# Optimization experiments

Hardware: AMD Instinct MI355X
Metric: run time of the kernel (lower is better)

The kernel has to match this reference:

```python
import jax, jax.numpy as jnp
import numpy as np

D_MODEL = 1024
N_HEADS = 16
HEAD_DIM = D_MODEL // N_HEADS


def setup_inputs() -> dict:
    key = jax.random.key(0)
    ks = jax.random.split(key, 5)
    s = 1.0 / np.sqrt(D_MODEL)
    return {
        "x": jax.random.normal(ks[0], (2, 2048, D_MODEL), dtype=jnp.float32),
        "w_qkv": jax.random.uniform(ks[1], (3 * D_MODEL, D_MODEL), jnp.float32, -s, s),
        "b_qkv": jax.random.uniform(ks[2], (3 * D_MODEL,), jnp.float32, -s, s),
        "w_out": jax.random.uniform(ks[3], (D_MODEL, D_MODEL), jnp.float32, -s, s),
        "b_out": jax.random.uniform(ks[4], (D_MODEL,), jnp.float32, -s, s),
    }


def _attn(x, w_qkv, b_qkv, w_out, b_out):
    bsz, seq_len, _ = x.shape
    qkv = jnp.einsum('bsd,ed->bse', x, w_qkv) + b_qkv  # [B,S,3D]
    q, k, v = jnp.split(qkv, 3, axis=-1)
    def heads(t):  # [B,S,D] -> [B,H,S,Dh]
        return t.reshape(bsz, seq_len, N_HEADS, HEAD_DIM).transpose(0, 2, 1, 3)
    q, k, v = heads(q), heads(k), heads(v)
    scores = jnp.einsum('bhqd,bhkd->bhqk', q, k) / np.sqrt(HEAD_DIM)
    mask = jnp.tril(jnp.ones((seq_len, seq_len), dtype=bool))
    scores = jnp.where(mask, scores, -jnp.inf)
    probs = jax.nn.softmax(scores, axis=-1)
    attn = jnp.einsum('bhqk,bhkd->bhqd', probs, v)
    attn = attn.transpose(0, 2, 1, 3).reshape(bsz, seq_len, D_MODEL)
    return jnp.einsum('bsd,ed->bse', attn, w_out) + b_out


def reference(x, w_qkv, b_qkv, w_out, b_out):
    return _attn(x, w_qkv, b_qkv, w_out, b_out)
```

## Files before the change

kernel.cpp:

```cpp
#include <hip/hip_runtime.h>
#include <hip/hip_bf16.h>
#include <stdint.h>

#define SEQ     2048
#define BATCH   2
#define NHEADS  16
#define HDIM    64
#define DMODEL  1024
#define N3      3072
#define D2      2048
#define MTOT    (BATCH*SEQ)

typedef __attribute__((ext_vector_type(4))) float f32x4;
typedef __attribute__((ext_vector_type(8))) short bf16x8;

static __device__ inline unsigned short f2bf(float f) {
    union { float f; unsigned u; } v; v.f = f;
    unsigned r = (v.u + 0x7fffu + ((v.u >> 16) & 1u)) >> 16;
    return (unsigned short)r;
}

#define GLDS(gp, lp) __builtin_amdgcn_global_load_lds( \
    (const __attribute__((address_space(1))) void*)(gp), \
    (__attribute__((address_space(3))) void*)(lp), 16, 0, 0)

__global__ void cast_all(const float* __restrict__ x,
                         const float* __restrict__ wqkv,
                         const float* __restrict__ wout,
                         unsigned short* __restrict__ xb,
                         unsigned short* __restrict__ wqkvb,
                         unsigned short* __restrict__ woutb) {
    long i4 = (long)(blockIdx.x * blockDim.x + threadIdx.x) * 4;
    const float* src; unsigned short* dst; long off;
    if (i4 < 4194304L)      { src = x;    dst = xb;    off = i4; }
    else if (i4 < 7340032L) { src = wqkv; dst = wqkvb; off = i4 - 4194304L; }
    else                    { src = wout; dst = woutb; off = i4 - 7340032L; }
    float4 v = *(const float4*)(src + off);
    ushort4 o;
    o.x = f2bf(v.x); o.y = f2bf(v.y); o.z = f2bf(v.z); o.w = f2bf(v.w);
    *(ushort4*)(dst + off) = o;
}

#define BK 32

__global__ __launch_bounds__(256, 2) void gemm_qkv(
    const unsigned short* __restrict__ A,
    const unsigned short* __restrict__ B,
    const float* __restrict__ bias,
    unsigned short* __restrict__ qk,
    unsigned short* __restrict__ vT)
{
    __shared__ __align__(16) unsigned short sA[2][128][BK];
    __shared__ __align__(16) unsigned short sB[2][128][BK];
    const int tid  = threadIdx.x;
    const int wave = tid >> 6, lane = tid & 63;
    const int quad = lane >> 4, l16 = lane & 15;
    const int wm = wave >> 1, wn = wave & 1;
    const int m0 = blockIdx.x * 128, n0 = blockIdx.y * 128;

    f32x4 acc[4][4];
    const f32x4 zero = {0.f, 0.f, 0.f, 0.f};
    #pragma unroll
    for (int i = 0; i < 4; i++)
        #pragma unroll
        for (int j = 0; j < 4; j++) acc[i][j] = zero;

    const unsigned short* gA0 = A + (long)(m0 + (tid >> 2)) * 1024 + (tid & 3) * 8;
    const unsigned short* gB0 = B + (long)(n0 + (tid >> 2)) * 1024 + (tid & 3) * 8;

    GLDS(gA0,               &sA[0][wave * 16][0]);
    GLDS(gA0 + 64L * 1024,  &sA[0][64 + wave * 16][0]);
    GLDS(gB0,               &sB[0][wave * 16][0]);
    GLDS(gB0 + 64L * 1024,  &sB[0][64 + wave * 16][0]);

    int buf = 0;
    for (int k0 = 0; k0 < 1024; k0 += BK, buf ^= 1) {
        __syncthreads();
        if (k0 + BK < 1024) {
            const unsigned short* ga = gA0 + k0 + BK;
            const unsigned short* gb = gB0 + k0 + BK;
            GLDS(ga,              &sA[buf ^ 1][wave * 16][0]);
            GLDS(ga + 64L * 1024, &sA[buf ^ 1][64 + wave * 16][0]);
            GLDS(gb,              &sB[buf ^ 1][wave * 16][0]);
            GLDS(gb + 64L * 1024, &sB[buf ^ 1][64 + wave * 16][0]);
        }
        bf16x8 af[4], bfr[4];
        #pragma unroll
        for (int mt = 0; mt < 4; mt++)
            af[mt] = *(const bf16x8*)(&sA[buf][wm * 64 + mt * 16 + l16][quad * 8]);
        #pragma unroll
        for (int nt = 0; nt < 4; nt++)
            bfr[nt] = *(const bf16x8*)(&sB[buf][wn * 64 + nt * 16 + l16][quad * 8]);
        #pragma unroll
        for (int mt = 0; mt < 4; mt++)
            #pragma unroll
            for (int nt = 0; nt < 4; nt++)
                acc[mt][nt] = __builtin_amdgcn_mfma_f32_16x16x32_bf16(
                    af[mt], bfr[nt], acc[mt][nt], 0, 0, 0);
    }

    if (n0 < 2048) {
        #pragma unroll
        for (int nt = 0; nt < 4; nt++) {
            const int n_g = n0 + wn * 64 + nt * 16 + l16;
            const float bv = bias[n_g];
            #pragma unroll
            for (int mt = 0; mt < 4; mt++) {
                #pragma unroll
                for (int r = 0; r < 4; r++) {
                    const int m_g = m0 + wm * 64 + mt * 16 + quad * 4 + r;
                    qk[(long)m_g * D2 + n_g] = f2bf(acc[mt][nt][r] + bv);
                }
            }
        }
    } else {
        const int b = m0 >> 11;
        #pragma unroll
        for (int nt = 0; nt < 4; nt++) {
            const int n_g = n0 + wn * 64 + nt * 16 + l16;
            const int dm = n_g - 2048;
            const long vrow = (long)(((b << 4) + (dm >> 6)) << 6) + (dm & 63);
            const float bv = bias[n_g];
            #pragma unroll
            for (int mt = 0; mt < 4; mt++) {
                const int m_g = m0 + wm * 64 + mt * 16 + quad * 4;
                ushort4 o;
                o.x = f2bf(acc[mt][nt][0] + bv);
                o.y = f2bf(acc[mt][nt][1] + bv);
                o.z = f2bf(acc[mt][nt][2] + bv);
                o.w = f2bf(acc[mt][nt][3] + bv);
                *(ushort4*)(vT + vrow * D2 + (m_g & 2047)) = o;
            }
        }
    }
}

__global__ __launch_bounds__(256, 2) void gemm_out(
    const unsigned short* __restrict__ A,
    const unsigned short* __restrict__ B,
    const float* __restrict__ bias,
    float* __restrict__ C)
{
    __shared__ __align__(16) unsigned short sA[2][128][BK];
    __shared__ __align__(16) unsigned short sB[2][64][BK];
    const int tid  = threadIdx.x;
    const int wave = tid >> 6, lane = tid & 63;
    const int quad = lane >> 4, l16 = lane & 15;
    const int wm = wave >> 1, wn = wave & 1;
    const int m0 = blockIdx.x * 128, n0 = blockIdx.y * 64;

    f32x4 acc[4][2];
    const f32x4 zero = {0.f, 0.f, 0.f, 0.f};
    #pragma unroll
    for (int i = 0; i < 4; i++) { acc[i][0] = zero; acc[i][1] = zero; }

    const unsigned short* gA0 = A + (long)(m0 + (tid >> 2)) * 1024 + (tid & 3) * 8;
    const unsigned short* gB0 = B + (long)(n0 + (tid >> 2)) * 1024 + (tid & 3) * 8;

    GLDS(gA0,              &sA[0][wave * 16][0]);
    GLDS(gA0 + 64L * 1024, &sA[0][64 + wave * 16][0]);
    GLDS(gB0,              &sB[0][wave * 16][0]);

    int buf = 0;
    for (int k0 = 0; k0 < 1024; k0 += BK, buf ^= 1) {
        __syncthreads();
        if (k0 + BK < 1024) {
            const unsigned short* ga = gA0 + k0 + BK;
            GLDS(ga,              &sA[buf ^ 1][wave * 16][0]);
            GLDS(ga + 64L * 1024, &sA[buf ^ 1][64 + wave * 16][0]);
            GLDS(gB0 + k0 + BK,   &sB[buf ^ 1][wave * 16][0]);
        }
        bf16x8 af[4], bfr[2];
        #pragma unroll
        for (int mt = 0; mt < 4; mt++)
            af[mt] = *(const bf16x8*)(&sA[buf][wm * 64 + mt * 16 + l16][quad * 8]);
        #pragma unroll
        for (int nt = 0; nt < 2; nt++)
            bfr[nt] = *(const bf16x8*)(&sB[buf][wn * 32 + nt * 16 + l16][quad * 8]);
        #pragma unroll
        for (int mt = 0; mt < 4; mt++)
            #pragma unroll
            for (int nt = 0; nt < 2; nt++)
                acc[mt][nt] = __builtin_amdgcn_mfma_f32_16x16x32_bf16(
                    af[mt], bfr[nt], acc[mt][nt], 0, 0, 0);
    }
    #pragma unroll
    for (int nt = 0; nt < 2; nt++) {
        const int n_g = n0 + wn * 32 + nt * 16 + l16;
        const float bv = bias[n_g];
        #pragma unroll
        for (int mt = 0; mt < 4; mt++) {
            #pragma unroll
            for (int r = 0; r < 4; r++) {
                const int m_g = m0 + wm * 64 + mt * 16 + quad * 4 + r;
                C[(long)m_g * DMODEL + n_g] = acc[mt][nt][r] + bv;
            }
        }
    }
}

__global__ __launch_bounds__(256, 2) void attn_kernel(
    const unsigned short* __restrict__ qk,
    const unsigned short* __restrict__ vT,
    unsigned short* __restrict__ attn)
{
    __shared__ __align__(16) unsigned short sK [2][64][64];
    __shared__ __align__(16) unsigned short sVt[2][64][64];
    __shared__ __align__(16) unsigned short sP [4][2][16][64];

    const int tid  = threadIdx.x;
    const int w    = tid >> 6, lane = tid & 63;
    const int quad = lane >> 4, l16 = lane & 15, l7 = l16 & 7;

    const int bh = blockIdx.x;
    const int b  = bh >> 4, h = bh & 15;
    const int qtile = 15 - (int)blockIdx.y;
    const int qbase = qtile * 128;
    const int ntiles = 2 * qtile + 2;
    const long rowb = (long)b * SEQ;

    bf16x8 qfr[2][2];
    #pragma unroll
    for (int qf = 0; qf < 2; qf++) {
        const int q = qbase + w * 32 + qf * 16 + l16;
        const unsigned short* qp = qk + (rowb + q) * D2 + h * HDIM;
        qfr[qf][0] = *(const bf16x8*)(qp + quad * 8);
        qfr[qf][1] = *(const bf16x8*)(qp + 32 + quad * 8);
    }

    const f32x4 zero = {0.f, 0.f, 0.f, 0.f};
    f32x4 Oacc[4][2];
    #pragma unroll
    for (int mf = 0; mf < 4; mf++) { Oacc[mf][0] = zero; Oacc[mf][1] = zero; }
    float m_i[2] = {-1e30f, -1e30f}, l_i[2] = {0.f, 0.f};

    const int rl = lane >> 3;
    const int sm = (lane & 7) ^ (rl & 7);
    const unsigned short* kg  = qk + (rowb + w * 16 + rl) * D2 + 1024 + h * HDIM + sm * 8;
    const unsigned short* kg2 = kg + 8L * D2;
    const unsigned short* vg  = vT + (long)(bh * 64 + w * 16 + rl) * D2 + sm * 8;
    const unsigned short* vg2 = vg + 8L * D2;

    GLDS(kg,  &sK [0][w * 16][0]);
    GLDS(kg2, &sK [0][w * 16 + 8][0]);
    GLDS(vg,  &sVt[0][w * 16][0]);
    GLDS(vg2, &sVt[0][w * 16 + 8][0]);

    const int s0 = quad ^ l7;
    const int wminrow = qbase + w * 32;
    const int wmaxrow = wminrow + 31;
    const float C2 = 0.18033688011112042f;

    int buf = 0;
    for (int t = 0; t < ntiles; ++t, buf ^= 1) {
        const int kv0 = t * 64;
        __syncthreads();
        if (t + 1 < ntiles) {
            const long offk = (long)(t + 1) * 64 * D2;
            const int  offv = (t + 1) * 64;
            GLDS(kg + offk,  &sK [buf ^ 1][w * 16][0]);
            GLDS(kg2 + offk, &sK [buf ^ 1][w * 16 + 8][0]);
            GLDS(vg + offv,  &sVt[buf ^ 1][w * 16][0]);
            GLDS(vg2 + offv, &sVt[buf ^ 1][w * 16 + 8][0]);
        }
        if (kv0 > wmaxrow) continue;

        f32x4 st[4][2];
        #pragma unroll
        for (int kvf = 0; kvf < 4; kvf++) {
            bf16x8 kf0 = *(const bf16x8*)(&sK[buf][kvf * 16 + l16][s0 * 8]);
            bf16x8 kf1 = *(const bf16x8*)(&sK[buf][kvf * 16 + l16][(s0 ^ 4) * 8]);
            #pragma unroll
            for (int qf = 0; qf < 2; qf++) {
                st[kvf][qf] = __builtin_amdgcn_mfma_f32_16x16x32_bf16(kf0, qfr[qf][0], zero, 0, 0, 0);
                st[kvf][qf] = __builtin_amdgcn_mfma_f32_16x16x32_bf16(kf1, qfr[qf][1], st[kvf][qf], 0, 0, 0);
            }
        }
        if (kv0 + 63 > wminrow) {
            #pragma unroll
            for (int qf = 0; qf < 2; qf++) {
                const int q = wminrow + qf * 16 + l16;
                #pragma unroll
                for (int kvf = 0; kvf < 4; kvf++) {
                    const int kv = kv0 + kvf * 16 + quad * 4;
                    #pragma unroll
                    for (int r = 0; r < 4; r++)
                        if (kv + r > q) st[kvf][qf][r] = -1e30f;
                }
            }
        }
        #pragma unroll
        for (int qf = 0; qf < 2; qf++) {
            f32x4 mv0, mv;
            #pragma unroll
            for (int r = 0; r < 4; r++) {
                mv0[r] = fmaxf(st[0][qf][r], st[1][qf][r]);
                mv[r]  = fmaxf(mv0[r], fmaxf(st[2][qf][r], st[3][qf][r]));
            }
            float mx = fmaxf(fmaxf(mv[0], mv[1]), fmaxf(mv[2], mv[3]));
            mx = fmaxf(mx, __shfl_xor(mx, 16));
            mx = fmaxf(mx, __shfl_xor(mx, 32));
            const float mnew  = fmaxf(m_i[qf], mx);
            const float alpha = __builtin_amdgcn_exp2f((m_i[qf] - mnew) * C2);
            const float cm    = mnew * C2;
            #pragma unroll
            for (int kvf = 0; kvf < 4; kvf++) {
                f32x4 a = st[kvf][qf] * C2 - cm;
                #pragma unroll
                for (int r = 0; r < 4; r++)
                    st[kvf][qf][r] = __builtin_amdgcn_exp2f(a[r]);
            }
            f32x4 ps = (st[0][qf] + st[1][qf]) + (st[2][qf] + st[3][qf]);
            l_i[qf] = l_i[qf] * alpha + ((ps[0] + ps[1]) + (ps[2] + ps[3]));
            m_i[qf] = mnew;
            #pragma unroll
            for (int mf = 0; mf < 4; mf++) Oacc[mf][qf] *= alpha;
            #pragma unroll
            for (int kvf = 0; kvf < 4; kvf++) {
                ushort4 o;
                o.x = f2bf(st[kvf][qf][0]); o.y = f2bf(st[kvf][qf][1]);
                o.z = f2bf(st[kvf][qf][2]); o.w = f2bf(st[kvf][qf][3]);
                const int seg = (kvf * 2 + (quad >> 1)) ^ l7;
                *(ushort4*)(&sP[w][qf][l16][seg * 8 + (quad & 1) * 4]) = o;
            }
        }
        bf16x8 pf[2][2];
        #pragma unroll
        for (int qf = 0; qf < 2; qf++)
            #pragma unroll
            for (int ks = 0; ks < 2; ks++)
                pf[qf][ks] = *(const bf16x8*)(&sP[w][qf][l16][((ks * 4 + quad) ^ l7) * 8]);
        #pragma unroll
        for (int mf = 0; mf < 4; mf++) {
            bf16x8 vf0 = *(const bf16x8*)(&sVt[buf][mf * 16 + l16][s0 * 8]);
            bf16x8 vf1 = *(const bf16x8*)(&sVt[buf][mf * 16 + l16][(s0 ^ 4) * 8]);
            #pragma unroll
            for (int qf = 0; qf < 2; qf++) {
                Oacc[mf][qf] = __builtin_amdgcn_mfma_f32_16x16x32_bf16(vf0, pf[qf][0], Oacc[mf][qf], 0, 0, 0);
                Oacc[mf][qf] = __builtin_amdgcn_mfma_f32_16x16x32_bf16(vf1, pf[qf][1], Oacc[mf][qf], 0, 0, 0);
            }
        }
    }
    #pragma unroll
    for (int qf = 0; qf < 2; qf++) {
        float L = l_i[qf];
        L += __shfl_xor(L, 16);
        L += __shfl_xor(L, 32);
        const float inv = 1.0f / L;
        const int q = qbase + w * 32 + qf * 16 + l16;
        unsigned short* op = attn + (rowb + q) * DMODEL + h * HDIM + quad * 4;
        #pragma unroll
        for (int mf = 0; mf < 4; mf++) {
            ushort4 o;
            o.x = f2bf(Oacc[mf][qf][0] * inv);
            o.y = f2bf(Oacc[mf][qf][1] * inv);
            o.z = f2bf(Oacc[mf][qf][2] * inv);
            o.w = f2bf(Oacc[mf][qf][3] * inv);
            *(ushort4*)(op + mf * 16) = o;
        }
    }
}

extern "C" void kernel_launch(void* const* d_in, const int* in_sizes, int n_in,
                              void* d_out, int out_size, void* d_ws, size_t ws_size,
                              hipStream_t stream) {
    const float* x    = (const float*)d_in[0];
    const float* wqkv = (const float*)d_in[1];
    const float* bqkv = (const float*)d_in[2];
    const float* wout = (const float*)d_in[3];
    const float* bout = (const float*)d_in[4];

    char* ws = (char*)d_ws;
    unsigned short* xb    = (unsigned short*)(ws);
    unsigned short* wqkvb = (unsigned short*)(ws + (8L << 20));
    unsigned short* woutb = (unsigned short*)(ws + (14L << 20));
    unsigned short* qkb   = (unsigned short*)(ws + (16L << 20));
    unsigned short* vTb   = (unsigned short*)(ws + (32L << 20));
    unsigned short* attnb = (unsigned short*)(ws + (40L << 20));

    cast_all<<<8192, 256, 0, stream>>>(x, wqkv, wout, xb, wqkvb, woutb);

    dim3 g1(32, 24);
    gemm_qkv<<<g1, 256, 0, stream>>>(xb, wqkvb, bqkv, qkb, vTb);

    dim3 g2(32, 16);
    attn_kernel<<<g2, 256, 0, stream>>>(qkb, vTb, attnb);

    dim3 g3(32, 16);
    gemm_out<<<g3, 256, 0, stream>>>(attnb, woutb, bout, (float*)d_out);
}
```

Before: 195.1 us.

## Pair causal query tiles per block and load two KV tiles per stage

Each attention block now processes two 64-row query tiles, one short and one long (pair and 31-pair), to balance the causal workload across blocks. Each warp owns 16 query rows instead of 32. K/V tiles are fetched in pairs into a double buffer, halving the number of barriers per tile. This costs less reuse of the K/V fragments per warp and more shared memory, which may reduce occupancy.

Result: faster. 186.1 us (-4.6%).

```diff
diff --git a/kernel.cpp b/kernel.cpp
--- a/kernel.cpp
+++ b/kernel.cpp
@@ -204,9 +204,9 @@
     const unsigned short* __restrict__ vT,
     unsigned short* __restrict__ attn)
 {
-    __shared__ __align__(16) unsigned short sK [2][64][64];
-    __shared__ __align__(16) unsigned short sVt[2][64][64];
-    __shared__ __align__(16) unsigned short sP [4][2][16][64];
+    __shared__ __align__(16) unsigned short sK [2][2][64][64];
+    __shared__ __align__(16) unsigned short sVt[2][2][64][64];
+    __shared__ __align__(16) unsigned short sP [4][16][64];
 
     const int tid  = threadIdx.x;
     const int w    = tid >> 6, lane = tid & 63;
@@ -214,148 +214,143 @@
 
     const int bh = blockIdx.x;
     const int b  = bh >> 4, h = bh & 15;
-    const int qtile = 15 - (int)blockIdx.y;
-    const int qbase = qtile * 128;
-    const int ntiles = 2 * qtile + 2;
+    const int pair = blockIdx.y;
     const long rowb = (long)b * SEQ;
 
-    bf16x8 qfr[2][2];
+    const int rl = lane >> 3;
+    const int sm = (lane & 7) ^ rl;
+    const unsigned short* kg = qk + (rowb + w * 16 + rl) * D2 + 1024 + h * HDIM + sm * 8;
+    const unsigned short* vg = vT + (long)(bh * 64 + w * 16 + rl) * D2 + sm * 8;
+
+    const int s0 = quad ^ l7;
+    const float C2 = 0.18033688011112042f;
+    const f32x4 zero = {0.f, 0.f, 0.f, 0.f};
+
     #pragma unroll
-    for (int qf = 0; qf < 2; qf++) {
-        const int q = qbase + w * 32 + qf * 16 + l16;
-        const unsigned short* qp = qk + (rowb + q) * D2 + h * HDIM;
-        qfr[qf][0] = *(const bf16x8*)(qp + quad * 8);
-        qfr[qf][1] = *(const bf16x8*)(qp + 32 + quad * 8);
-    }
-
-    const f32x4 zero = {0.f, 0.f, 0.f, 0.f};
-    f32x4 Oacc[4][2];
-    #pragma unroll
-    for (int mf = 0; mf < 4; mf++) { Oacc[mf][0] = zero; Oacc[mf][1] = zero; }
-    float m_i[2] = {-1e30f, -1e30f}, l_i[2] = {0.f, 0.f};
-
-    const int rl = lane >> 3;
-    const int sm = (lane & 7) ^ (rl & 7);
-    const unsigned short* kg  = qk + (rowb + w * 16 + rl) * D2 + 1024 + h * HDIM + sm * 8;
-    const unsigned short* kg2 = kg + 8L * D2;
-    const unsigned short* vg  = vT + (long)(bh * 64 + w * 16 + rl) * D2 + sm * 8;
-    const unsigned short* vg2 = vg + 8L * D2;
-
-    GLDS(kg,  &sK [0][w * 16][0]);
-    GLDS(kg2, &sK [0][w * 16 + 8][0]);
-    GLDS(vg,  &sVt[0][w * 16][0]);
-    GLDS(vg2, &sVt[0][w * 16 + 8][0]);
-
-    const int s0 = quad ^ l7;
-    const int wminrow = qbase + w * 32;
-    const int wmaxrow = wminrow + 31;
-    const float C2 = 0.18033688011112042f;
-
-    int buf = 0;
-    for (int t = 0; t < ntiles; ++t, buf ^= 1) {
-        const int kv0 = t * 64;
+    for (int ph = 0; ph < 2; ph++) {
+        const int qtile  = ph ? (31 - pair) : pair;
+        const int qbase  = qtile * 64;
+        const int ntiles = qtile + 1;
+        const int npairs = (ntiles + 1) >> 1;
+
+        bf16x8 qf0, qf1;
+        {
+            const unsigned short* qp = qk + (rowb + qbase + w * 16 + l16) * D2 + h * HDIM;
+            qf0 = *(const bf16x8*)(qp + quad * 8);
+            qf1 = *(const bf16x8*)(qp + 32 + quad * 8);
+        }
+        f32x4 Oacc[4];
+        #pragma unroll
+        for (int mf = 0; mf < 4; mf++) Oacc[mf] = zero;
+        float m_i = -1e30f, l_i = 0.f;
+
         __syncthreads();
-        if (t + 1 < ntiles) {
-            const long offk = (long)(t + 1) * 64 * D2;
-            const int  offv = (t + 1) * 64;
-            GLDS(kg + offk,  &sK [buf ^ 1][w * 16][0]);
-            GLDS(kg2 + offk, &sK [buf ^ 1][w * 16 + 8][0]);
-            GLDS(vg + offv,  &sVt[buf ^ 1][w * 16][0]);
-            GLDS(vg2 + offv, &sVt[buf ^ 1][w * 16 + 8][0]);
-        }
-        if (kv0 > wmaxrow) continue;
-
-        f32x4 st[4][2];
-        #pragma unroll
-        for (int kvf = 0; kvf < 4; kvf++) {
-            bf16x8 kf0 = *(const bf16x8*)(&sK[buf][kvf * 16 + l16][s0 * 8]);
-            bf16x8 kf1 = *(const bf16x8*)(&sK[buf][kvf * 16 + l16][(s0 ^ 4) * 8]);
-            #pragma unroll
-            for (int qf = 0; qf < 2; qf++) {
-                st[kvf][qf] = __builtin_amdgcn_mfma_f32_16x16x32_bf16(kf0, qfr[qf][0], zero, 0, 0, 0);
-                st[kvf][qf] = __builtin_amdgcn_mfma_f32_16x16x32_bf16(kf1, qfr[qf][1], st[kvf][qf], 0, 0, 0);
-            }
-        }
-        if (kv0 + 63 > wminrow) {
-            #pragma unroll
-            for (int qf = 0; qf < 2; qf++) {
-                const int q = wminrow + qf * 16 + l16;
+        {
+            const long o0 = 0, o1 = (long)(1 <= qtile ? 1 : qtile) * 64;
+            GLDS(kg + o0 * D2,           &sK [0][0][w * 16][0]);
+            GLDS(kg + o0 * D2 + 8L * D2, &sK [0][0][w * 16 + 8][0]);
+            GLDS(vg + o0,                &sVt[0][0][w * 16][0]);
+            GLDS(vg + o0 + 8L * D2,      &sVt[0][0][w * 16 + 8][0]);
+            GLDS(kg + o1 * D2,           &sK [0][1][w * 16][0]);
+            GLDS(kg + o1 * D2 + 8L * D2, &sK [0][1][w * 16 + 8][0]);
+            GLDS(vg + o1,                &sVt[0][1][w * 16][0]);
+            GLDS(vg + o1 + 8L * D2,      &sVt[0][1][w * 16 + 8][0]);
+        }
+
+        int buf = 0;
+        for (int p = 0; p < npairs; p++, buf ^= 1) {
+            __syncthreads();
+            if (p + 1 < npairs) {
+                const int t0 = 2 * p + 2, t1 = 2 * p + 3;
+                const long o0 = (long)(t0 <= qtile ? t0 : qtile) * 64;
+                const long o1 = (long)(t1 <= qtile ? t1 : qtile) * 64;
+                GLDS(kg + o0 * D2,           &sK [buf ^ 1][0][w * 16][0]);
+                GLDS(kg + o0 * D2 + 8L * D2, &sK [buf ^ 1][0][w * 16 + 8][0]);
+                GLDS(vg + o0,                &sVt[buf ^ 1][0][w * 16][0]);
+                GLDS(vg + o0 + 8L * D2,      &sVt[buf ^ 1][0][w * 16 + 8][0]);
+                GLDS(kg + o1 * D2,           &sK [buf ^ 1][1][w * 16][0]);
+                GLDS(kg + o1 * D2 + 8L * D2, &sK [buf ^ 1][1][w * 16 + 8][0]);
+                GLDS(vg + o1,                &sVt[buf ^ 1][1][w * 16][0]);
+                GLDS(vg + o1 + 8L * D2,      &sVt[buf ^ 1][1][w * 16 + 8][0]);
+            }
+            #pragma unroll
+            for (int s = 0; s < 2; s++) {
+                const int t = 2 * p + s;
+                if (t >= ntiles) break;
+
+                f32x4 st[4];
                 #pragma unroll
                 for (int kvf = 0; kvf < 4; kvf++) {
-                    const int kv = kv0 + kvf * 16 + quad * 4;
+                    bf16x8 kf0 = *(const bf16x8*)(&sK[buf][s][kvf * 16 + l16][s0 * 8]);
+                    bf16x8 kf1 = *(const bf16x8*)(&sK[buf][s][kvf * 16 + l16][(s0 ^ 4) * 8]);
+                    st[kvf] = __builtin_amdgcn_mfma_f32_16x16x32_bf16(kf0, qf0, zero, 0, 0, 0);
+                    st[kvf] = __builtin_amdgcn_mfma_f32_16x16x32_bf16(kf1, qf1, st[kvf], 0, 0, 0);
+                }
+                if (t == qtile) {
+                    const int ql = w * 16 + l16;
+                    #pragma unroll
+                    for (int kvf = 0; kvf < 4; kvf++) {
+                        const int kv = kvf * 16 + quad * 4;
+                        #pragma unroll
+                        for (int r = 0; r < 4; r++)
+                            if (kv + r > ql) st[kvf][r] = -1e30f;
+                    }
+                }
+                f32x4 mv;
+                #pragma unroll
+                for (int r = 0; r < 4; r++)
+                    mv[r] = fmaxf(fmaxf(st[0][r], st[1][r]), fmaxf(st[2][r], st[3][r]));
+                float mx = fmaxf(fmaxf(mv[0], mv[1]), fmaxf(mv[2], mv[3]));
+                mx = fmaxf(mx, __shfl_xor(mx, 16));
+                mx = fmaxf(mx, __shfl_xor(mx, 32));
+                const float mnew  = fmaxf(m_i, mx);
+                const float alpha = __builtin_amdgcn_exp2f((m_i - mnew) * C2);
+                const float cm    = mnew * C2;
+                #pragma unroll
+                for (int kvf = 0; kvf < 4; kvf++) {
+                    f32x4 a = st[kvf] * C2 - cm;
                     #pragma unroll
                     for (int r = 0; r < 4; r++)
-                        if (kv + r > q) st[kvf][qf][r] = -1e30f;
-                }
-            }
-        }
-        #pragma unroll
-        for (int qf = 0; qf < 2; qf++) {
-            f32x4 mv0, mv;
-            #pragma unroll
-            for (int r = 0; r < 4; r++) {
-                mv0[r] = fmaxf(st[0][qf][r], st[1][qf][r]);
-                mv[r]  = fmaxf(mv0[r], fmaxf(st[2][qf][r], st[3][qf][r]));
-            }
-            float mx = fmaxf(fmaxf(mv[0], mv[1]), fmaxf(mv[2], mv[3]));
-            mx = fmaxf(mx, __shfl_xor(mx, 16));
-            mx = fmaxf(mx, __shfl_xor(mx, 32));
-            const float mnew  = fmaxf(m_i[qf], mx);
-            const float alpha = __builtin_amdgcn_exp2f((m_i[qf] - mnew) * C2);
-            const float cm    = mnew * C2;
-            #pragma unroll
-            for (int kvf = 0; kvf < 4; kvf++) {
-                f32x4 a = st[kvf][qf] * C2 - cm;
-                #pragma unroll
-                for (int r = 0; r < 4; r++)
-                    st[kvf][qf][r] = __builtin_amdgcn_exp2f(a[r]);
-            }
-            f32x4 ps = (st[0][qf] + st[1][qf]) + (st[2][qf] + st[3][qf]);
-            l_i[qf] = l_i[qf] * alpha + ((ps[0] + ps[1]) + (ps[2] + ps[3]));
-            m_i[qf] = mnew;
-            #pragma unroll
-            for (int mf = 0; mf < 4; mf++) Oacc[mf][qf] *= alpha;
-            #pragma unroll
-            for (int kvf = 0; kvf < 4; kvf++) {
-                ushort4 o;
-                o.x = f2bf(st[kvf][qf][0]); o.y = f2bf(st[kvf][qf][1]);
-                o.z = f2bf(st[kvf][qf][2]); o.w = f2bf(st[kvf][qf][3]);
-                const int seg = (kvf * 2 + (quad >> 1)) ^ l7;
-                *(ushort4*)(&sP[w][qf][l16][seg * 8 + (quad & 1) * 4]) = o;
-            }
-        }
-        bf16x8 pf[2][2];
-        #pragma unroll
-        for (int qf = 0; qf < 2; qf++)
-            #pragma unroll
-            for (int ks = 0; ks < 2; ks++)
-                pf[qf][ks] = *(const bf16x8*)(&sP[w][qf][l16][((ks * 4 + quad) ^ l7) * 8]);
-        #pragma unroll
-        for (int mf = 0; mf < 4; mf++) {
-            bf16x8 vf0 = *(const bf16x8*)(&sVt[buf][mf * 16 + l16][s0 * 8]);
-            bf16x8 vf1 = *(const bf16x8*)(&sVt[buf][mf * 16 + l16][(s0 ^ 4) * 8]);
-            #pragma unroll
-            for (int qf = 0; qf < 2; qf++) {
-                Oacc[mf][qf] = __builtin_amdgcn_mfma_f32_16x16x32_bf16(vf0, pf[qf][0], Oacc[mf][qf], 0, 0, 0);
-                Oacc[mf][qf] = __builtin_amdgcn_mfma_f32_16x16x32_bf16(vf1, pf[qf][1], Oacc[mf][qf], 0, 0, 0);
-            }
-        }
-    }
-    #pragma unroll
-    for (int qf = 0; qf < 2; qf++) {
-        float L = l_i[qf];
+                        st[kvf][r] = __builtin_amdgcn_exp2f(a[r]);
+                }
+                f32x4 ps = (st[0] + st[1]) + (st[2] + st[3]);
+                l_i = l_i * alpha + ((ps[0] + ps[1]) + (ps[2] + ps[3]));
+                m_i = mnew;
+                #pragma unroll
+                for (int mf = 0; mf < 4; mf++) Oacc[mf] *= alpha;
+
+                #pragma unroll
+                for (int kvf = 0; kvf < 4; kvf++) {
+                    ushort4 o;
+                    o.x = f2bf(st[kvf][0]); o.y = f2bf(st[kvf][1]);
+                    o.z = f2bf(st[kvf][2]); o.w = f2bf(st[kvf][3]);
+                    const int seg = (kvf * 2 + (quad >> 1)) ^ l7;
+                    *(ushort4*)(&sP[w][l16][seg * 8 + (quad & 1) * 4]) = o;
+                }
+                bf16x8 pf0 = *(const bf16x8*)(&sP[w][l16][((quad) ^ l7) * 8]);
+                bf16x8 pf1 = *(const bf16x8*)(&sP[w][l16][((4 + quad) ^ l7) * 8]);
+                #pragma unroll
+                for (int mf = 0; mf < 4; mf++) {
+                    bf16x8 vf0 = *(const bf16x8*)(&sVt[buf][s][mf * 16 + l16][s0 * 8]);
+                    bf16x8 vf1 = *(const bf16x8*)(&sVt[buf][s][mf * 16 + l16][(s0 ^ 4) * 8]);
+                    Oacc[mf] = __builtin_amdgcn_mfma_f32_16x16x32_bf16(vf0, pf0, Oacc[mf], 0, 0, 0);
+                    Oacc[mf] = __builtin_amdgcn_mfma_f32_16x16x32_bf16(vf1, pf1, Oacc[mf], 0, 0, 0);
+                }
+            }
+        }
+        float L = l_i;
         L += __shfl_xor(L, 16);
         L += __shfl_xor(L, 32);
         const float inv = 1.0f / L;
-        const int q = qbase + w * 32 + qf * 16 + l16;
+        const int q = qbase + w * 16 + l16;
         unsigned short* op = attn + (rowb + q) * DMODEL + h * HDIM + quad * 4;
         #pragma unroll
         for (int mf = 0; mf < 4; mf++) {
             ushort4 o;
-            o.x = f2bf(Oacc[mf][qf][0] * inv);
-            o.y = f2bf(Oacc[mf][qf][1] * inv);
-            o.z = f2bf(Oacc[mf][qf][2] * inv);
-            o.w = f2bf(Oacc[mf][qf][3] * inv);
+            o.x = f2bf(Oacc[mf][0] * inv);
+            o.y = f2bf(Oacc[mf][1] * inv);
+            o.z = f2bf(Oacc[mf][2] * inv);
+            o.w = f2bf(Oacc[mf][3] * inv);
             *(ushort4*)(op + mf * 16) = o;
         }
     }
```

## Split attention into 64-row query tiles with 2-wave blocks and paired scheduling

Applied to the files above, without the earlier changes.

The attention kernel now uses 128-thread blocks, each handling a 64-row query tile instead of 128 rows with 4 waves, and the grid doubles to 32x32. Query tiles are interleaved long and short (31-y/2 alternating with y/2) to balance causal work across blocks. Each wave now loads 32 KV rows per tile, and the per-wave skip of fully masked tiles is dropped because the tile shape makes it unnecessary. This removes idle waves on the diagonal and improves load balance, but halves K/V reuse per block, so global and LDS traffic per query rises.

New measurement: 210.2 us. +7.8%, slower.

```diff
diff --git a/kernel.cpp b/kernel.cpp
--- a/kernel.cpp
+++ b/kernel.cpp
@@ -199,14 +199,14 @@
     }
 }
 
-__global__ __launch_bounds__(256, 2) void attn_kernel(
+__global__ __launch_bounds__(128) void attn_kernel(
     const unsigned short* __restrict__ qk,
     const unsigned short* __restrict__ vT,
     unsigned short* __restrict__ attn)
 {
     __shared__ __align__(16) unsigned short sK [2][64][64];
     __shared__ __align__(16) unsigned short sVt[2][64][64];
-    __shared__ __align__(16) unsigned short sP [4][2][16][64];
+    __shared__ __align__(16) unsigned short sP [2][2][16][64];
 
     const int tid  = threadIdx.x;
     const int w    = tid >> 6, lane = tid & 63;
@@ -214,16 +214,16 @@
 
     const int bh = blockIdx.x;
     const int b  = bh >> 4, h = bh & 15;
-    const int qtile = 15 - (int)blockIdx.y;
-    const int qbase = qtile * 128;
-    const int ntiles = 2 * qtile + 2;
+    const int y  = blockIdx.y;
+    const int qtile = (y & 1) ? (y >> 1) : (31 - (y >> 1));
+    const int qbase = qtile * 64;
+    const int ntiles = qtile + 1;
     const long rowb = (long)b * SEQ;
 
     bf16x8 qfr[2][2];
     #pragma unroll
     for (int qf = 0; qf < 2; qf++) {
-        const int q = qbase + w * 32 + qf * 16 + l16;
-        const unsigned short* qp = qk + (rowb + q) * D2 + h * HDIM;
+        const unsigned short* qp = qk + (rowb + qbase + w * 32 + qf * 16 + l16) * D2 + h * HDIM;
         qfr[qf][0] = *(const bf16x8*)(qp + quad * 8);
         qfr[qf][1] = *(const bf16x8*)(qp + 32 + quad * 8);
     }
@@ -235,35 +235,31 @@
     float m_i[2] = {-1e30f, -1e30f}, l_i[2] = {0.f, 0.f};
 
     const int rl = lane >> 3;
-    const int sm = (lane & 7) ^ (rl & 7);
-    const unsigned short* kg  = qk + (rowb + w * 16 + rl) * D2 + 1024 + h * HDIM + sm * 8;
-    const unsigned short* kg2 = kg + 8L * D2;
-    const unsigned short* vg  = vT + (long)(bh * 64 + w * 16 + rl) * D2 + sm * 8;
-    const unsigned short* vg2 = vg + 8L * D2;
-
-    GLDS(kg,  &sK [0][w * 16][0]);
-    GLDS(kg2, &sK [0][w * 16 + 8][0]);
-    GLDS(vg,  &sVt[0][w * 16][0]);
-    GLDS(vg2, &sVt[0][w * 16 + 8][0]);
+    const int sm = (lane & 7) ^ rl;
+    const unsigned short* kg = qk + (rowb + w * 32 + rl) * D2 + 1024 + h * HDIM + sm * 8;
+    const unsigned short* vg = vT + (long)(bh * 64 + w * 32 + rl) * D2 + sm * 8;
 
     const int s0 = quad ^ l7;
-    const int wminrow = qbase + w * 32;
-    const int wmaxrow = wminrow + 31;
     const float C2 = 0.18033688011112042f;
+
+    #pragma unroll
+    for (int i = 0; i < 4; i++) {
+        GLDS(kg + (long)(8 * i) * D2, &sK [0][w * 32 + 8 * i][0]);
+        GLDS(vg + (long)(8 * i) * D2, &sVt[0][w * 32 + 8 * i][0]);
+    }
 
     int buf = 0;
     for (int t = 0; t < ntiles; ++t, buf ^= 1) {
-        const int kv0 = t * 64;
         __syncthreads();
         if (t + 1 < ntiles) {
             const long offk = (long)(t + 1) * 64 * D2;
             const int  offv = (t + 1) * 64;
-            GLDS(kg + offk,  &sK [buf ^ 1][w * 16][0]);
-            GLDS(kg2 + offk, &sK [buf ^ 1][w * 16 + 8][0]);
-            GLDS(vg + offv,  &sVt[buf ^ 1][w * 16][0]);
-            GLDS(vg2 + offv, &sVt[buf ^ 1][w * 16 + 8][0]);
-        }
-        if (kv0 > wmaxrow) continue;
+            #pragma unroll
+            for (int i = 0; i < 4; i++) {
+                GLDS(kg + offk + (long)(8 * i) * D2, &sK [buf ^ 1][w * 32 + 8 * i][0]);
+                GLDS(vg + offv + (long)(8 * i) * D2, &sVt[buf ^ 1][w * 32 + 8 * i][0]);
+            }
+        }
 
         f32x4 st[4][2];
         #pragma unroll
@@ -276,27 +272,26 @@
                 st[kvf][qf] = __builtin_amdgcn_mfma_f32_16x16x32_bf16(kf1, qfr[qf][1], st[kvf][qf], 0, 0, 0);
             }
         }
-        if (kv0 + 63 > wminrow) {
+        if (t == qtile) {
             #pragma unroll
             for (int qf = 0; qf < 2; qf++) {
-                const int q = wminrow + qf * 16 + l16;
+                const int ql = w * 32 + qf * 16 + l16;
                 #pragma unroll
                 for (int kvf = 0; kvf < 4; kvf++) {
-                    const int kv = kv0 + kvf * 16 + quad * 4;
+                    const int kv = kvf * 16 + quad * 4;
                     #pragma unroll
                     for (int r = 0; r < 4; r++)
-                        if (kv + r > q) st[kvf][qf][r] = -1e30f;
+                        if (kv + r > ql) st[kvf][qf][r] = -1e30f;
                 }
             }
         }
         #pragma unroll
         for (int qf = 0; qf < 2; qf++) {
-            f32x4 mv0, mv;
-            #pragma unroll
-            for (int r = 0; r < 4; r++) {
-                mv0[r] = fmaxf(st[0][qf][r], st[1][qf][r]);
-                mv[r]  = fmaxf(mv0[r], fmaxf(st[2][qf][r], st[3][qf][r]));
-            }
+            f32x4 mv;
+            #pragma unroll
+            for (int r = 0; r < 4; r++)
+                mv[r] = fmaxf(fmaxf(st[0][qf][r], st[1][qf][r]),
+                              fmaxf(st[2][qf][r], st[3][qf][r]));
             float mx = fmaxf(fmaxf(mv[0], mv[1]), fmaxf(mv[2], mv[3]));
             mx = fmaxf(mx, __shfl_xor(mx, 16));
             mx = fmaxf(mx, __shfl_xor(mx, 32));
@@ -326,10 +321,10 @@
         }
         bf16x8 pf[2][2];
         #pragma unroll
-        for (int qf = 0; qf < 2; qf++)
-            #pragma unroll
-            for (int ks = 0; ks < 2; ks++)
-                pf[qf][ks] = *(const bf16x8*)(&sP[w][qf][l16][((ks * 4 + quad) ^ l7) * 8]);
+        for (int qf = 0; qf < 2; qf++) {
+            pf[qf][0] = *(const bf16x8*)(&sP[w][qf][l16][(quad ^ l7) * 8]);
+            pf[qf][1] = *(const bf16x8*)(&sP[w][qf][l16][((4 + quad) ^ l7) * 8]);
+        }
         #pragma unroll
         for (int mf = 0; mf < 4; mf++) {
             bf16x8 vf0 = *(const bf16x8*)(&sVt[buf][mf * 16 + l16][s0 * 8]);
@@ -383,8 +378,8 @@
     dim3 g1(32, 24);
     gemm_qkv<<<g1, 256, 0, stream>>>(xb, wqkvb, bqkv, qkb, vTb);
 
-    dim3 g2(32, 16);
-    attn_kernel<<<g2, 256, 0, stream>>>(qkb, vTb, attnb);
+    dim3 g2(32, 32);
+    attn_kernel<<<g2, 128, 0, stream>>>(qkb, vTb, attnb);
 
     dim3 g3(32, 16);
     gemm_out<<<g3, 256, 0, stream>>>(attnb, woutb, bout, (float*)d_out);
```
